# Kernel optimization log

Measured on AMD Instinct MI355X. Metric: run time of the kernel, lower is better.

Reference implementation:

```python
import jax, jax.numpy as jnp
import numpy as np
from jax import lax


def setup_inputs() -> dict:
    key = jax.random.key(0)
    k1, k2 = jax.random.split(key)
    B, E, C = 8192, 256, 25
    encodings = jax.random.normal(k1, (B, E), dtype=jnp.float32)
    categorical = jax.random.uniform(k2, (B, C), dtype=jnp.float32)
    return {"encodings": encodings, "categorical": categorical, "k": 15}


def reference(encodings, categorical, k):
    # hard cluster assignment per sample: [B]
    hard_groups = jnp.argmax(categorical, axis=1)
    n_components = categorical.shape[1]

    # pairwise Euclidean distances [B, B] via the GEMM-based cdist identity
    sq = jnp.sum(encodings * encodings, axis=1)                    # [B]
    d2 = sq[:, None] + sq[None, :] - 2.0 * (encodings @ encodings.T)
    dists = jnp.sqrt(jnp.maximum(d2, 0.0))                          # [B, B]

    # k-th smallest distance per row (tf: tf.gather(tf.sort(distances), k))
    neg_topk, _ = lax.top_k(-dists, k + 1)                          # [B, k+1]
    thresh = -neg_topk[:, k]                                        # [B]

    # strict neighbourhood mask (tf: distances < max_distance)
    mask = (dists < thresh[:, None]).astype(jnp.float32)            # [B, B]

    # per-row histogram of neighbour cluster labels via one-hot GEMM
    onehot = jax.nn.one_hot(hard_groups, n_components, dtype=jnp.float32)  # [B, C]
    counts = mask @ onehot                                          # [B, C]
    n_neigh = jnp.sum(mask, axis=1, keepdims=True)                  # [B, 1]
    bins = counts / n_neigh
    # zero-count bins contribute 0 * log(1e-5) = 0, matching tf.bincount semantics
    neighbourhood_entropy = -jnp.sum(bins * jnp.log(bins + 1e-5), axis=1)  # [B]

    # layer's call returns encodings (identity); entropy is the metric being kernel-optimized
    return encodings, neighbourhood_entropy
```

## Files before the change

kernel.cpp:

```cpp
#include <hip/hip_runtime.h>
#include <cstdint>
#include <cstring>
#include <cstddef>

#define B 8192
#define E 256
#define C 25
#define K 15

#define RB 64
#define NCHUNK 4
#define CCHUNK (B/NCHUNK)
#define CT 64
#define NTILES (CCHUNK/CT)
#define NLISTS 64
#define NREF 32

typedef short bf16x8 __attribute__((ext_vector_type(8)));
typedef float f32x16 __attribute__((ext_vector_type(16)));

union U16 { uint4 u; bf16x8 h; };

static __device__ __forceinline__ unsigned short f2bf(float f) {
    unsigned u; __builtin_memcpy(&u, &f, 4);
    u += 0x7fffu + ((u >> 16) & 1u);
    return (unsigned short)(u >> 16);
}
static __device__ __forceinline__ unsigned pack2(float a, float b) {
    return (unsigned)f2bf(a) | ((unsigned)f2bf(b) << 16);
}
static __device__ __forceinline__ unsigned umn(unsigned a, unsigned b) { return a < b ? a : b; }
static __device__ __forceinline__ unsigned umx(unsigned a, unsigned b) { return a > b ? a : b; }

static __device__ __forceinline__ void gload_lds16(const void* g, void* l) {
    __builtin_amdgcn_global_load_lds(
        (const __attribute__((address_space(1))) void*)g,
        (__attribute__((address_space(3))) void*)l, 16, 0, 0);
}

__global__ __launch_bounds__(64) void prep_kernel(
    const float* __restrict__ enc, const float* __restrict__ cat,
    float* __restrict__ out, float* __restrict__ sqg, int* __restrict__ lab,
    unsigned short* __restrict__ bfb)
{
    const int row  = blockIdx.x;
    const int lane = threadIdx.x;

    const float4 v = ((const float4*)(enc + (size_t)row * E))[lane];
    ((float4*)(out + (size_t)row * E))[lane] = v;

    uint2 p; p.x = pack2(v.x, v.y); p.y = pack2(v.z, v.w);
    ((uint2*)(bfb + (size_t)row * E))[lane] = p;

    float s = v.x * v.x + v.y * v.y + v.z * v.z + v.w * v.w;
    #pragma unroll
    for (int off = 32; off; off >>= 1) s += __shfl_xor(s, off);
    if (lane == 0) sqg[row] = s;

    float cv = (lane < C) ? cat[(size_t)row * C + lane] : -1e30f;
    int   ci = lane;
    #pragma unroll
    for (int off = 32; off; off >>= 1) {
        float ov = __shfl_xor(cv, off);
        int   oi = __shfl_xor(ci, off);
        if (ov > cv || (ov == cv && oi < ci)) { cv = ov; ci = oi; }
    }
    if (lane == 0) lab[row] = ci;
}

__global__ __launch_bounds__(256, 2) void dist_topk_kernel(
    const unsigned short* __restrict__ bfb, const float* __restrict__ sqg,
    float2* __restrict__ cand)
{
    __shared__ char smem[50176];
    uint4* lB            = (uint4*)smem;
    unsigned (*lD)[68]   = (unsigned(*)[68])(smem + 32768);
    unsigned* dumpD      = (unsigned*)smem;

    const int tid  = threadIdx.x;
    const int lane = tid & 63, wv = tid >> 6;
    const int wr = wv >> 1, wc = wv & 1;
    const int hg = lane >> 5;
    const int sr = tid >> 2, qq = tid & 3;
    const int r0 = blockIdx.x * RB;
    const int cbase = blockIdx.y * CCHUNK;

    #define STAGE_B(c0_)                                                       \
        {                                                                      \
            _Pragma("unroll")                                                  \
            for (int i = 0; i < 8; ++i) {                                      \
                const int kc = wv * 8 + i;                                     \
                const int c  = lane ^ (kc & 7);                                \
                gload_lds16(bfb + (size_t)((c0_) + c) * E + kc * 8,            \
                            (char*)smem + (size_t)kc * 1024);                  \
            }                                                                  \
        }

    bf16x8 afrag[16];
    const int arow = r0 + wr * 32 + (lane & 31);
    {
        const uint4* src = (const uint4*)(bfb + (size_t)arow * E);
        #pragma unroll
        for (int s = 0; s < 16; ++s) { U16 t; t.u = src[s * 2 + hg]; afrag[s] = t.h; }
    }
    float srw[16];
    #pragma unroll
    for (int r = 0; r < 16; ++r) {
        const int rl = wr * 32 + (r & 3) + 8 * (r >> 2) + 4 * hg;
        srw[r] = sqg[r0 + rl];
    }

    const int cl = wc * 32 + (lane & 31);
    const unsigned paylane = (unsigned)(cl & 15);

    unsigned td[16];
    #pragma unroll
    for (int i = 0; i < 16; ++i) td[i] = 0xFFFFFFFFu;

    STAGE_B(cbase);

    #pragma clang loop unroll(disable)
    for (int ct = 0; ct < NTILES; ++ct) {
        const int c0 = cbase + ct * CT;
        __syncthreads();

        const float sc = sqg[c0 + cl];

        f32x16 acc;
        #pragma unroll
        for (int i = 0; i < 16; ++i) acc[i] = 0.f;
        #pragma unroll
        for (int s = 0; s < 16; ++s) {
            const int kc = s * 2 + hg;
            U16 t; t.u = lB[kc * 64 + (cl ^ (kc & 7))];
            acc = __builtin_amdgcn_mfma_f32_32x32x16_bf16(afrag[s], t.h, acc, 0, 0, 0);
        }
        const unsigned payt = ((unsigned)ct << 4) | paylane;
        #pragma unroll
        for (int r = 0; r < 16; ++r) {
            const int rl = wr * 32 + (r & 3) + 8 * (r >> 2) + 4 * hg;
            const float d2 = fmaxf(fmaf(-2.f, acc[r], srw[r] + sc), 0.f);
            unsigned bits; __builtin_memcpy(&bits, &d2, 4);
            lD[rl][cl] = (bits & 0xFFFFFE00u) | payt;
        }
        __syncthreads();

        if (ct + 1 < NTILES) STAGE_B(c0 + CT);

        unsigned nv[16];
        {
            const uint4* rowp = (const uint4*)(&lD[sr][qq * 16]);
            #pragma unroll
            for (int q4 = 0; q4 < 4; ++q4) {
                const uint4 u = rowp[q4];
                nv[q4*4+0] = u.x; nv[q4*4+1] = u.y; nv[q4*4+2] = u.z; nv[q4*4+3] = u.w;
            }
        }
        #pragma unroll
        for (int k = 2; k <= 16; k <<= 1) {
            #pragma unroll
            for (int j = k >> 1; j > 0; j >>= 1) {
                #pragma unroll
                for (int i = 0; i < 16; ++i) {
                    const int l = i ^ j;
                    if (l > i) {
                        const unsigned a = nv[i], b = nv[l];
                        if ((i & k) == 0) { nv[i] = umn(a, b); nv[l] = umx(a, b); }
                        else             { nv[i] = umx(a, b); nv[l] = umn(a, b); }
                    }
                }
            }
        }
        unsigned m2[16];
        #pragma unroll
        for (int i = 0; i < 16; ++i) m2[i] = umn(td[i], nv[15 - i]);
        #pragma unroll
        for (int j = 8; j > 0; j >>= 1) {
            #pragma unroll
            for (int i = 0; i < 16; ++i) {
                if ((i & j) == 0) {
                    const unsigned a = m2[i], b = m2[i | j];
                    m2[i] = umn(a, b); m2[i | j] = umx(a, b);
                }
            }
        }
        #pragma unroll
        for (int i = 0; i < 16; ++i) td[i] = m2[i];
    }

    __syncthreads();
    #pragma unroll
    for (int i = 0; i < 16; ++i) dumpD[tid * 16 + i] = td[i];
    __syncthreads();

    if (tid < RB) {
        int p0 = 0, p1 = 0, p2 = 0, p3 = 0;
        const int base = tid * 4 * 16;
        float2* outp = cand + (size_t)(r0 + tid) * NLISTS + blockIdx.y * 16;
        for (int o = 0; o < 16; ++o) {
            const unsigned h0 = dumpD[base + 0*16 + p0];
            const unsigned h1 = dumpD[base + 1*16 + p1];
            const unsigned h2 = dumpD[base + 2*16 + p2];
            const unsigned h3 = dumpD[base + 3*16 + p3];
            unsigned bd = h0; int bq = 0;
            if (h1 < bd) { bd = h1; bq = 1; }
            if (h2 < bd) { bd = h2; bq = 2; }
            if (h3 < bd) { bd = h3; bq = 3; }
            const int col = cbase + (int)((bd >> 4) & 31) * CT + bq * 16 + (int)(bd & 15);
            outp[o] = make_float2(__uint_as_float(bd & 0xFFFFFE00u), __int_as_float(col));
            if (bq == 0) ++p0; else if (bq == 1) ++p1; else if (bq == 2) ++p2; else ++p3;
        }
    }
    #undef STAGE_B
}

__global__ __launch_bounds__(128) void entropy_kernel(
    const float4* __restrict__ enc4, const float2* __restrict__ cand,
    const int* __restrict__ lab, float* __restrict__ out)
{
    __shared__ float part[2][NREF][68];
    __shared__ int   colbuf[2][NREF];
    const int lane = threadIdx.x & 63;
    const int wid  = threadIdx.x >> 6;
    const int row  = blockIdx.x * 2 + wid;

    const float4 rv = enc4[(size_t)row * 64 + lane];
    const float2 cd = cand[(size_t)row * NLISTS + lane];
    const int mycol = __float_as_int(cd.y);
    unsigned mykey; __builtin_memcpy(&mykey, &cd.x, 4);

    int ar = 0;
    for (int m = 0; m < 64; ++m) {
        const unsigned km = __shfl(mykey, m);
        ar += (km < mykey || (km == mykey && m < lane)) ? 1 : 0;
    }
    if (ar < NREF) colbuf[wid][ar] = mycol;
    __syncthreads();

    #pragma unroll 4
    for (int m = 0; m < NREF; ++m) {
        const int cm = colbuf[wid][m];
        const float4 cv = enc4[(size_t)cm * 64 + lane];
        const float dx = rv.x - cv.x, dy = rv.y - cv.y;
        const float dz = rv.z - cv.z, dw = rv.w - cv.w;
        part[wid][m][lane] = dx * dx + dy * dy + dz * dz + dw * dw;
    }
    __syncthreads();

    const int ocol = colbuf[wid][lane & (NREF - 1)];
    double a = 1.0e300;
    if (lane < NREF) {
        a = 0.0;
        const float4* pr = (const float4*)&part[wid][lane][0];
        #pragma unroll
        for (int j = 0; j < 16; ++j) {
            const float4 p = pr[j];
            a += (double)p.x + (double)p.y + (double)p.z + (double)p.w;
        }
    }

    int rank = 0;
    for (int m = 0; m < 64; ++m) {
        const double dm = __shfl(a, m);
        rank += (dm < a || (dm == a && m < lane)) ? 1 : 0;
    }
    const unsigned long long b15 = __ballot(rank == K);
    const int tl = __ffsll((unsigned long long)b15) - 1;
    const double thresh = __shfl(a, tl);

    const bool act = (a < thresh);
    const int n = __popcll(__ballot(act));
    const int myval = act ? lab[ocol] : -1;

    int cnt = 0;
    for (int m = 0; m < 64; ++m) cnt += (__shfl(myval, m) == lane) ? 1 : 0;

    float H = 0.f;
    if (lane < C && n > 0) {
        const float bins = (float)cnt / (float)n;
        H = -bins * logf(bins + 1e-5f);
    }
    #pragma unroll
    for (int off = 32; off; off >>= 1) H += __shfl_xor(H, off);
    if (lane == 0) out[(size_t)B * E + row] = H;
}

extern "C" void kernel_launch(void* const* d_in, const int* in_sizes, int n_in,
                              void* d_out, int out_size, void* d_ws, size_t ws_size,
                              hipStream_t stream)
{
    (void)in_sizes; (void)n_in; (void)out_size; (void)ws_size;
    const float* enc = (const float*)d_in[0];
    const float* cat = (const float*)d_in[1];
    float*  out  = (float*)d_out;
    float*  sqg  = (float*)d_ws;
    int*    lab  = ((int*)d_ws) + B;
    float2* cand = (float2*)((char*)d_ws + (size_t)2 * B * 4);
    unsigned short* bfb =
        (unsigned short*)((char*)d_ws + (size_t)2 * B * 4 + (size_t)B * NLISTS * 8);

    prep_kernel<<<B, 64, 0, stream>>>(enc, cat, out, sqg, lab, bfb);
    dist_topk_kernel<<<dim3(B / RB, NCHUNK), 256, 0, stream>>>(bfb, sqg, cand);
    entropy_kernel<<<B / 2, 128, 0, stream>>>((const float4*)enc, cand, lab, out);
}
```

Before: 223.9 us.

## Split column range into 8 chunks and pack candidate key with column index

The distance/top-k kernel now splits columns into 8 chunks instead of 4, doubling the grid to raise parallelism, with each chunk writing 16 candidates per row. Candidates are packed into one 32-bit word (truncated distance key in the high bits, 13-bit column in the low bits), halving the bytes per candidate so total candidate traffic stays the same. The entropy kernel ranks 128 candidates with two per lane and trims later shuffle loops to 32 iterations. Keeping more mantissa bits cleared could add ties near the threshold, although exact fp64 refinement over the top 32 should cover that.

```diff
diff --git a/kernel.cpp b/kernel.cpp
--- a/kernel.cpp
+++ b/kernel.cpp
@@ -9,11 +9,11 @@
 #define K 15
 
 #define RB 64
-#define NCHUNK 4
+#define NCHUNK 8
 #define CCHUNK (B/NCHUNK)
 #define CT 64
 #define NTILES (CCHUNK/CT)
-#define NLISTS 64
+#define NLISTS 128
 #define NREF 32
 
 typedef short bf16x8 __attribute__((ext_vector_type(8)));
@@ -70,7 +70,7 @@
 
 __global__ __launch_bounds__(256, 2) void dist_topk_kernel(
     const unsigned short* __restrict__ bfb, const float* __restrict__ sqg,
-    float2* __restrict__ cand)
+    unsigned* __restrict__ cand)
 {
     __shared__ char smem[50176];
     uint4* lB            = (uint4*)smem;
@@ -196,7 +196,7 @@
     if (tid < RB) {
         int p0 = 0, p1 = 0, p2 = 0, p3 = 0;
         const int base = tid * 4 * 16;
-        float2* outp = cand + (size_t)(r0 + tid) * NLISTS + blockIdx.y * 16;
+        unsigned* outp = cand + (size_t)(r0 + tid) * NLISTS + blockIdx.y * 16;
         for (int o = 0; o < 16; ++o) {
             const unsigned h0 = dumpD[base + 0*16 + p0];
             const unsigned h1 = dumpD[base + 1*16 + p1];
@@ -207,7 +207,7 @@
             if (h2 < bd) { bd = h2; bq = 2; }
             if (h3 < bd) { bd = h3; bq = 3; }
             const int col = cbase + (int)((bd >> 4) & 31) * CT + bq * 16 + (int)(bd & 15);
-            outp[o] = make_float2(__uint_as_float(bd & 0xFFFFFE00u), __int_as_float(col));
+            outp[o] = (bd & 0xFFFFE000u) | (unsigned)col;
             if (bq == 0) ++p0; else if (bq == 1) ++p1; else if (bq == 2) ++p2; else ++p3;
         }
     }
@@ -215,7 +215,7 @@
 }
 
 __global__ __launch_bounds__(128) void entropy_kernel(
-    const float4* __restrict__ enc4, const float2* __restrict__ cand,
+    const float4* __restrict__ enc4, const unsigned* __restrict__ cand,
     const int* __restrict__ lab, float* __restrict__ out)
 {
     __shared__ float part[2][NREF][68];
@@ -225,19 +225,23 @@
     const int row  = blockIdx.x * 2 + wid;
 
     const float4 rv = enc4[(size_t)row * 64 + lane];
-    const float2 cd = cand[(size_t)row * NLISTS + lane];
-    const int mycol = __float_as_int(cd.y);
-    unsigned mykey; __builtin_memcpy(&mykey, &cd.x, 4);
-
-    int ar = 0;
+    const uint2 kk = ((const uint2*)(cand + (size_t)row * NLISTS))[lane];
+    const unsigned k0 = kk.x, k1 = kk.y;
+
+    int r0n = 0, r1n = 0;
     for (int m = 0; m < 64; ++m) {
-        const unsigned km = __shfl(mykey, m);
-        ar += (km < mykey || (km == mykey && m < lane)) ? 1 : 0;
-    }
-    if (ar < NREF) colbuf[wid][ar] = mycol;
+        const unsigned a0 = __shfl(k0, m);
+        const unsigned a1 = __shfl(k1, m);
+        r0n += (a0 < k0 || (a0 == k0 && m <  lane)) ? 1 : 0;
+        r0n += (a1 < k0 || (a1 == k0 && m <  lane)) ? 1 : 0;
+        r1n += (a0 < k1 || (a0 == k1 && m <= lane)) ? 1 : 0;
+        r1n += (a1 < k1 || (a1 == k1 && m <  lane)) ? 1 : 0;
+    }
+    if (r0n < NREF) colbuf[wid][r0n] = (int)(k0 & 8191u);
+    if (r1n < NREF) colbuf[wid][r1n] = (int)(k1 & 8191u);
     __syncthreads();
 
-    #pragma unroll 4
+    #pragma unroll 8
     for (int m = 0; m < NREF; ++m) {
         const int cm = colbuf[wid][m];
         const float4 cv = enc4[(size_t)cm * 64 + lane];
@@ -260,7 +264,7 @@
     }
 
     int rank = 0;
-    for (int m = 0; m < 64; ++m) {
+    for (int m = 0; m < NREF; ++m) {
         const double dm = __shfl(a, m);
         rank += (dm < a || (dm == a && m < lane)) ? 1 : 0;
     }
@@ -273,7 +277,7 @@
     const int myval = act ? lab[ocol] : -1;
 
     int cnt = 0;
-    for (int m = 0; m < 64; ++m) cnt += (__shfl(myval, m) == lane) ? 1 : 0;
+    for (int m = 0; m < NREF; ++m) cnt += (__shfl(myval, m) == lane) ? 1 : 0;
 
     float H = 0.f;
     if (lane < C && n > 0) {
@@ -292,12 +296,12 @@
     (void)in_sizes; (void)n_in; (void)out_size; (void)ws_size;
     const float* enc = (const float*)d_in[0];
     const float* cat = (const float*)d_in[1];
-    float*  out  = (float*)d_out;
-    float*  sqg  = (float*)d_ws;
-    int*    lab  = ((int*)d_ws) + B;
-    float2* cand = (float2*)((char*)d_ws + (size_t)2 * B * 4);
+    float*    out  = (float*)d_out;
+    float*    sqg  = (float*)d_ws;
+    int*      lab  = ((int*)d_ws) + B;
+    unsigned* cand = (unsigned*)((char*)d_ws + (size_t)2 * B * 4);
     unsigned short* bfb =
-        (unsigned short*)((char*)d_ws + (size_t)2 * B * 4 + (size_t)B * NLISTS * 8);
+        (unsigned short*)((char*)d_ws + (size_t)2 * B * 4 + (size_t)B * NLISTS * 4);
 
     prep_kernel<<<B, 64, 0, stream>>>(enc, cat, out, sqg, lab, bfb);
     dist_topk_kernel<<<dim3(B / RB, NCHUNK), 256, 0, stream>>>(bfb, sqg, cand);
```

Result: slower. 230.3 us (+2.8%).
